# Performance work log

Measured on AMD Instinct MI355X. Metric: run time of the kernel, lower is better.

## Reference

```python
import jax, jax.numpy as jnp
import numpy as np

ROBOT_W = 1.0
PHASE_W = 1.0
COHER_W = 10.0
SPEED_W = 5.0
MAX_SPEED = 10.0
SMOOTH_VEL_W = 0.05
SMOOTH_ACC_W = 0.01

# illegal phase transitions {(0,2),(1,0),(2,0),(2,1)} as a 3x3 lookup table
_ILLEGAL = np.zeros((3, 3), dtype=bool)
for a, b in [(0, 2), (1, 0), (2, 0), (2, 1)]:
    _ILLEGAL[a, b] = True
ILLEGAL_TABLE = jnp.asarray(_ILLEGAL)


def setup_inputs() -> dict:
    key = jax.random.key(0)
    k1, k2, k3, k4 = jax.random.split(key, 4)
    B, T = 256, 8192
    # scale by 8 so per-frame speeds (norm of diffs of 3-vectors) exceed MAX_SPEED
    pred_robot = jax.random.normal(k1, (B, T, 12), dtype=jnp.float32) * 8.0
    gt_robot = jax.random.normal(k2, (B, T, 12), dtype=jnp.float32) * 8.0
    pred_phase = jax.random.normal(k3, (B, T, 3), dtype=jnp.float32)
    gt_phase = jax.random.randint(k4, (B, T), 0, 3, dtype=jnp.int32)
    return {"pred_robot": pred_robot, "pred_phase": pred_phase,
            "gt_robot": gt_robot, "gt_phase": gt_phase}


def _coherence_loss(phase_logits):
    # vectorized replacement for the O(B*T) Python double loop
    p = jnp.argmax(phase_logits, axis=-1)            # [B, T]
    pt, pt1 = p[:, :-1], p[:, 1:]                    # [B, T-1]
    illegal = ILLEGAL_TABLE[pt, pt1]                 # [B, T-1] bool
    # logit of the (illegal) predicted phase at t+1
    sel = jnp.take_along_axis(phase_logits[:, 1:], pt1[..., None], axis=-1)[..., 0]
    loss_sum = jnp.sum(jnp.where(illegal, sel * sel, 0.0))
    count = jnp.sum(illegal)
    return jnp.where(count > 0, loss_sum / jnp.maximum(count, 1).astype(sel.dtype), 0.0)


def _speed_loss(pred_robot):
    B, T, D = pred_robot.shape
    vel = pred_robot[:, 1:] - pred_robot[:, :-1]     # [B, T-1, 12]
    pts = vel.reshape(B, T - 1, 4, 3)
    speeds = jnp.linalg.norm(pts, axis=-1)           # [B, T-1, 4]
    pen = jax.nn.relu(speeds - MAX_SPEED)
    return SPEED_W * jnp.mean(pen * pen)


def reference(pred_robot, pred_phase, gt_robot, gt_phase):
    # MSE over robot trajectory
    robot_loss = jnp.mean((pred_robot - gt_robot) ** 2)
    # cross-entropy over 3 phase classes
    logp = jax.nn.log_softmax(pred_phase, axis=-1)   # [B, T, 3]
    nll = -jnp.take_along_axis(logp, gt_phase[..., None].astype(jnp.int32), axis=-1)[..., 0]
    phase_loss = jnp.mean(nll)
    coherence = _coherence_loss(pred_phase)
    speed_loss = _speed_loss(pred_robot)
    vel = pred_robot[:, 1:] - pred_robot[:, :-1]
    vel_loss = jnp.mean(vel * vel)
    acc = pred_robot[:, 2:] - 2.0 * pred_robot[:, 1:-1] + pred_robot[:, :-2]
    acc_loss = jnp.mean(acc * acc)
    total = (ROBOT_W * robot_loss + PHASE_W * phase_loss + COHER_W * coherence
             + speed_loss + SMOOTH_VEL_W * vel_loss + SMOOTH_ACC_W * acc_loss)
    return total
```

## Files before the change

### kernel.cpp

```cpp
#include <hip/hip_runtime.h>
#include <math.h>

#define B_DIM 256
#define T_DIM 8192
#define BLOCK 256
#define NSLOT 256
#define K_PRED 4
#define NPB (BLOCK * K_PRED)
#define NF4 (B_DIM * T_DIM * 3)
#define NPH4 (NF4 / 4)
#define GRID_BLOCKS (NF4 / NPB)


__device__ __forceinline__ unsigned div3u(unsigned x) {
    return __umulhi(x, 0xAAAAAAABu) >> 1;
}
__device__ __forceinline__ float pen_term(float s) {
    float d = fmaxf(sqrtf(s) - 10.0f, 0.0f);
    return d * d;
}
__device__ __forceinline__ void argmax3(float l0, float l1, float l2, int &p, float &m) {
    p = 0; m = l0;
    if (l1 > m) { m = l1; p = 1; }
    if (l2 > m) { m = l2; p = 2; }
}
__device__ __forceinline__ float nll3(float l0, float l1, float l2, int g) {
    float mx = fmaxf(l0, fmaxf(l1, l2));
    float lse = mx + logf(expf(l0 - mx) + expf(l1 - mx) + expf(l2 - mx));
    float sel = (g == 0) ? l0 : ((g == 1) ? l1 : l2);
    return lse - sel;
}

__global__ __launch_bounds__(BLOCK) void combined_loss_main(
    const float4* __restrict__ pred4,
    const float4* __restrict__ ph4,
    const float4* __restrict__ gt4,
    const int*    __restrict__ gt_phase,
    double* __restrict__ ws)
{
    __shared__ float  s_carry[NPB + 1];
    __shared__ float2 s_zw[BLOCK + 1];
    __shared__ float  s_pm_m[BLOCK + 1];
    __shared__ int    s_pm_p[BLOCK + 1];
    __shared__ float  s_red[4][6];

    const int tid = threadIdx.x;
    const int blk = blockIdx.x;
    const unsigned base = (unsigned)blk * NPB;

    float sse = 0.f, velsq = 0.f, accsq = 0.f;
    float loc[K_PRED], car[K_PRED];
    unsigned c0v = 0;

    #pragma unroll
    for (int k = 0; k < K_PRED; ++k) {
        const unsigned i = base + (unsigned)(k * BLOCK) + tid;
        const unsigned r = div3u(i);
        const unsigned c = i - 3u * r;
        if (k == 0) c0v = c;
        const unsigned t = r & (T_DIM - 1);
        const bool v1 = t < (T_DIM - 1);
        const bool v2 = t < (T_DIM - 2);
        const unsigned i3 = v1 ? i + 3u : i;
        const unsigned i6 = v2 ? i + 6u : i;

        const float4 A  = pred4[i];
        const float4 G  = gt4[i];
        const float4 A3 = pred4[i3];
        const float4 A6 = pred4[i6];

        float d;
        d = A.x - G.x; sse = fmaf(d, d, sse);
        d = A.y - G.y; sse = fmaf(d, d, sse);
        d = A.z - G.z; sse = fmaf(d, d, sse);
        d = A.w - G.w; sse = fmaf(d, d, sse);

        float sqx = 0.f, sqy = 0.f, sqz = 0.f, sqw = 0.f;
        if (v1) {
            const float vx = A3.x - A.x, vy = A3.y - A.y, vz = A3.z - A.z, vw = A3.w - A.w;
            sqx = vx * vx; sqy = vy * vy; sqz = vz * vz; sqw = vw * vw;
            velsq += sqx + sqy + sqz + sqw;
        }
        if (v2) {
            float a;
            a = A6.x - 2.0f * A3.x + A.x; accsq = fmaf(a, a, accsq);
            a = A6.y - 2.0f * A3.y + A.y; accsq = fmaf(a, a, accsq);
            a = A6.z - 2.0f * A3.z + A.z; accsq = fmaf(a, a, accsq);
            a = A6.w - 2.0f * A3.w + A.w; accsq = fmaf(a, a, accsq);
        }
        float l3v, crv;
        if (c == 0)      { l3v = sqx + sqy + sqz; crv = sqw; }
        else if (c == 1) { l3v = sqz + sqw;       crv = sqx + sqy; }
        else             { l3v = sqy + sqz + sqw; crv = sqx; }
        loc[k] = l3v; car[k] = crv;
        s_carry[k * BLOCK + tid] = crv;
    }

    const unsigned j = (unsigned)blk * BLOCK + tid;
    const float4 P = ph4[j];
    s_zw[tid + 1] = make_float2(P.z, P.w);

    if (tid == 0) {
        float2 zwp = make_float2(0.f, 0.f);
        if (j != 0) {
            const float2* ph2 = (const float2*)ph4;
            zwp = ph2[2u * j - 1u];
        }
        s_zw[0] = zwp;
        float crs = 0.f;
        const unsigned ib = base + NPB;
        if (ib < (unsigned)NF4) {
            const unsigned rb = div3u(ib);
            const unsigned cb = ib - 3u * rb;
            const unsigned tb = rb & (T_DIM - 1);
            if (tb < (T_DIM - 1)) {
                const float4 Ab  = pred4[ib];
                const float4 Ab3 = pred4[ib + 3u];
                const float bx = Ab3.x - Ab.x, by = Ab3.y - Ab.y;
                const float bz = Ab3.z - Ab.z, bw = Ab3.w - Ab.w;
                const float sx = bx * bx, sy = by * by, sx2 = bz * bz, sw = bw * bw;
                (void)sx2;
                crs = (cb == 0) ? sw : ((cb == 1) ? (sx + sy) : sx);
            }
        }
        s_carry[NPB] = crs;
    }
    __syncthreads();

    const unsigned g   = div3u(j);
    const unsigned dph = j - 3u * g;
    const float2 zwp = s_zw[tid];
    float l0, l1, l2;
    if (dph == 0)      { l0 = P.x;   l1 = P.y;   l2 = P.z; }
    else if (dph == 1) { l0 = zwp.y; l1 = P.x;   l2 = P.y; }
    else               { l0 = zwp.x; l1 = zwp.y; l2 = P.x; }
    const unsigned prow = 4u * g + dph;

    int gA, gB = 0;
    if (dph == 2) {
        const int2 gg = ((const int2*)gt_phase)[prow >> 1];
        gA = gg.x; gB = gg.y;
    } else {
        gA = gt_phase[prow];
    }
    float nll = nll3(l0, l1, l2, gA);
    int pP; float mP;
    argmax3(l0, l1, l2, pP, mP);
    s_pm_m[tid] = mP; s_pm_p[tid] = pP;

    int p3 = 0; float m3 = 0.f;
    if (dph == 2) {
        nll += nll3(P.y, P.z, P.w, gB);
        argmax3(P.y, P.z, P.w, p3, m3);
    }
    if (tid == BLOCK - 1) {
        float mS = 0.f; int pS = 0;
        const unsigned jn = j + 1u;
        if (jn < (unsigned)NPH4) {
            const float4 Pn = ph4[jn];
            const unsigned gn = div3u(jn);
            const unsigned dn = jn - 3u * gn;
            float a0, a1, a2;
            if (dn == 0)      { a0 = Pn.x; a1 = Pn.y; a2 = Pn.z; }
            else if (dn == 1) { a0 = P.w;  a1 = Pn.x; a2 = Pn.y; }
            else              { a0 = P.z;  a1 = P.w;  a2 = Pn.x; }
            argmax3(a0, a1, a2, pS, mS);
        }
        s_pm_m[BLOCK] = mS; s_pm_p[BLOCK] = pS;
    }
    __syncthreads();

    float csum = 0.f, ccnt = 0.f;
    {
        const float mN = s_pm_m[tid + 1];
        const int   pN = s_pm_p[tid + 1];
        const unsigned t1 = prow & (T_DIM - 1);
        if (t1 < (T_DIM - 1)) {
            const int   pB2 = (dph == 2) ? p3 : pN;
            const float mB2 = (dph == 2) ? m3 : mN;
            const int mask = (pP == 0) ? 4 : ((pP == 1) ? 1 : 3);
            if ((mask >> pB2) & 1) { csum += mB2 * mB2; ccnt += 1.f; }
        }
        if (dph == 2) {
            const unsigned t2 = (prow + 1u) & (T_DIM - 1);
            if (t2 < (T_DIM - 1)) {
                const int mask = (p3 == 0) ? 4 : ((p3 == 1) ? 1 : 3);
                if ((mask >> pN) & 1) { csum += mN * mN; ccnt += 1.f; }
            }
        }
    }

    float pen2 = 0.f;
    #pragma unroll
    for (int k = 0; k < K_PRED; ++k) {
        unsigned ck = c0v + (unsigned)k;
        if (ck >= 3u) ck -= 3u;
        const float up = s_carry[k * BLOCK + tid + 1];
        const float a = loc[k] + ((ck == 1u) ? up : 0.f);
        const float b = (ck == 0u) ? (car[k] + up) : 0.f;
        pen2 += pen_term(a) + pen_term(b);
    }

    float vals[6] = { fmaf(12.0f, nll, sse), csum, ccnt, pen2, velsq, accsq };
    #pragma unroll
    for (int off = 32; off > 0; off >>= 1) {
        #pragma unroll
        for (int q = 0; q < 6; ++q)
            vals[q] += __shfl_down(vals[q], off, 64);
    }
    const int wave = tid >> 6, lane = tid & 63;
    if (lane == 0) {
        #pragma unroll
        for (int q = 0; q < 6; ++q) s_red[wave][q] = vals[q];
    }
    __syncthreads();
    if (tid < 6) {
        const double acc = (double)s_red[0][tid] + (double)s_red[1][tid]
                         + (double)s_red[2][tid] + (double)s_red[3][tid];
        atomicAdd(&ws[(size_t)(blk & (NSLOT - 1)) * 8 + tid], acc);
    }
}

__global__ __launch_bounds__(256) void combined_loss_final(
    const double* __restrict__ ws, float* __restrict__ out)
{
    __shared__ double sred[4][6];
    const int tid = threadIdx.x;
    double v[6];
    #pragma unroll
    for (int q = 0; q < 6; ++q) v[q] = ws[(size_t)tid * 8 + q];
    #pragma unroll
    for (int off = 32; off > 0; off >>= 1) {
        #pragma unroll
        for (int q = 0; q < 6; ++q)
            v[q] += __shfl_down(v[q], off, 64);
    }
    const int wave = tid >> 6, lane = tid & 63;
    if (lane == 0) {
        #pragma unroll
        for (int q = 0; q < 6; ++q) sred[wave][q] = v[q];
    }
    __syncthreads();
    if (tid == 0) {
        double s[6];
        #pragma unroll
        for (int q = 0; q < 6; ++q)
            s[q] = sred[0][q] + sred[1][q] + sred[2][q] + sred[3][q];
        const double robot_phase = s[0] / (double)((size_t)B_DIM * T_DIM * 12);
        const double coher = (s[2] > 0.0) ? (s[1] / fmax(s[2], 1.0)) : 0.0;
        const double speed = 5.0  * (s[3] / (double)((size_t)B_DIM * (T_DIM - 1) * 4));
        const double vel   = 0.05 * (s[4] / (double)((size_t)B_DIM * (T_DIM - 1) * 12));
        const double acc   = 0.01 * (s[5] / (double)((size_t)B_DIM * (T_DIM - 2) * 12));
        out[0] = (float)(robot_phase + 10.0 * coher + speed + vel + acc);
    }
}

extern "C" void kernel_launch(void* const* d_in, const int* in_sizes, int n_in,
                              void* d_out, int out_size, void* d_ws, size_t ws_size,
                              hipStream_t stream)
{
    const float4* pred4      = (const float4*)d_in[0];
    const float4* ph4        = (const float4*)d_in[1];
    const float4* gt4        = (const float4*)d_in[2];
    const int*    gt_phase   = (const int*)d_in[3];
    double* ws  = (double*)d_ws;
    float*  out = (float*)d_out;

    hipMemsetAsync(d_ws, 0, (size_t)NSLOT * 8 * sizeof(double), stream);

    combined_loss_main<<<dim3(GRID_BLOCKS), BLOCK, 0, stream>>>(pred4, ph4, gt4, gt_phase, ws);
    combined_loss_final<<<1, 256, 0, stream>>>(ws, out);
}
```

Measured before the change: 241.9 us.

## Hoist all global loads ahead of compute and use fast exp/log intrinsics

Restructures the main kernel so every global load (prediction, ground truth, shifted neighbours, phase logits, boundary carry and next-phase values) is issued up front into register arrays before any arithmetic. This aims to increase memory-level parallelism and hide load latency. It also swaps expf/logf for __expf/__logf in the cross-entropy and adds a min-blocks-per-SM hint of 3 to launch_bounds. The cost is higher register pressure from holding 16 float4 values live, plus slightly lower precision in the log-sum-exp.

```diff
diff --git a/kernel.cpp b/kernel.cpp
--- a/kernel.cpp
+++ b/kernel.cpp
@@ -26,12 +26,12 @@
 }
 __device__ __forceinline__ float nll3(float l0, float l1, float l2, int g) {
     float mx = fmaxf(l0, fmaxf(l1, l2));
-    float lse = mx + logf(expf(l0 - mx) + expf(l1 - mx) + expf(l2 - mx));
+    float s = __expf(l0 - mx) + __expf(l1 - mx) + __expf(l2 - mx);
     float sel = (g == 0) ? l0 : ((g == 1) ? l1 : l2);
-    return lse - sel;
-}
-
-__global__ __launch_bounds__(BLOCK) void combined_loss_main(
+    return mx + __logf(s) - sel;
+}
+
+__global__ __launch_bounds__(BLOCK, 3) void combined_loss_main(
     const float4* __restrict__ pred4,
     const float4* __restrict__ ph4,
     const float4* __restrict__ gt4,
@@ -47,95 +47,54 @@
     const int tid = threadIdx.x;
     const int blk = blockIdx.x;
     const unsigned base = (unsigned)blk * NPB;
-
-    float sse = 0.f, velsq = 0.f, accsq = 0.f;
-    float loc[K_PRED], car[K_PRED];
-    unsigned c0v = 0;
-
+    const unsigned j = (unsigned)blk * BLOCK + tid;
+
+
+    float2 zwp_s = make_float2(0.f, 0.f);
+    float4 Ab = make_float4(0.f,0.f,0.f,0.f), Ab3 = Ab;
+    unsigned cb = 0; bool carry_sent = false;
+    if (tid == 0) {
+        if (j != 0) zwp_s = ((const float2*)ph4)[2u * j - 1u];
+        const unsigned ib = base + NPB;
+        if (ib < (unsigned)NF4) {
+            const unsigned rb = div3u(ib);
+            cb = ib - 3u * rb;
+            if ((rb & (T_DIM - 1)) < (T_DIM - 1)) {
+                carry_sent = true;
+                Ab  = pred4[ib];
+                Ab3 = pred4[ib + 3u];
+            }
+        }
+    }
+    float4 Pn = make_float4(0.f,0.f,0.f,0.f);
+    bool pn_valid = false;
+    if (tid == BLOCK - 1) {
+        if (j + 1u < (unsigned)NPH4) { pn_valid = true; Pn = ph4[j + 1u]; }
+    }
+
+    float4 A[K_PRED], G[K_PRED], A3[K_PRED], A6[K_PRED];
+    unsigned cc[K_PRED];
+    bool vv1[K_PRED], vv2[K_PRED];
     #pragma unroll
     for (int k = 0; k < K_PRED; ++k) {
         const unsigned i = base + (unsigned)(k * BLOCK) + tid;
         const unsigned r = div3u(i);
-        const unsigned c = i - 3u * r;
-        if (k == 0) c0v = c;
+        cc[k] = i - 3u * r;
         const unsigned t = r & (T_DIM - 1);
-        const bool v1 = t < (T_DIM - 1);
-        const bool v2 = t < (T_DIM - 2);
-        const unsigned i3 = v1 ? i + 3u : i;
-        const unsigned i6 = v2 ? i + 6u : i;
-
-        const float4 A  = pred4[i];
-        const float4 G  = gt4[i];
-        const float4 A3 = pred4[i3];
-        const float4 A6 = pred4[i6];
-
-        float d;
-        d = A.x - G.x; sse = fmaf(d, d, sse);
-        d = A.y - G.y; sse = fmaf(d, d, sse);
-        d = A.z - G.z; sse = fmaf(d, d, sse);
-        d = A.w - G.w; sse = fmaf(d, d, sse);
-
-        float sqx = 0.f, sqy = 0.f, sqz = 0.f, sqw = 0.f;
-        if (v1) {
-            const float vx = A3.x - A.x, vy = A3.y - A.y, vz = A3.z - A.z, vw = A3.w - A.w;
-            sqx = vx * vx; sqy = vy * vy; sqz = vz * vz; sqw = vw * vw;
-            velsq += sqx + sqy + sqz + sqw;
-        }
-        if (v2) {
-            float a;
-            a = A6.x - 2.0f * A3.x + A.x; accsq = fmaf(a, a, accsq);
-            a = A6.y - 2.0f * A3.y + A.y; accsq = fmaf(a, a, accsq);
-            a = A6.z - 2.0f * A3.z + A.z; accsq = fmaf(a, a, accsq);
-            a = A6.w - 2.0f * A3.w + A.w; accsq = fmaf(a, a, accsq);
-        }
-        float l3v, crv;
-        if (c == 0)      { l3v = sqx + sqy + sqz; crv = sqw; }
-        else if (c == 1) { l3v = sqz + sqw;       crv = sqx + sqy; }
-        else             { l3v = sqy + sqz + sqw; crv = sqx; }
-        loc[k] = l3v; car[k] = crv;
-        s_carry[k * BLOCK + tid] = crv;
-    }
-
-    const unsigned j = (unsigned)blk * BLOCK + tid;
+        vv1[k] = t < (T_DIM - 1);
+        vv2[k] = t < (T_DIM - 2);
+        const unsigned ia = vv1[k] ? i + 3u : i;
+        const unsigned ic = vv2[k] ? i + 6u : i;
+        A[k]  = pred4[i];
+        G[k]  = gt4[i];
+        A3[k] = pred4[ia];
+        A6[k] = pred4[ic];
+    }
+
     const float4 P = ph4[j];
-    s_zw[tid + 1] = make_float2(P.z, P.w);
-
-    if (tid == 0) {
-        float2 zwp = make_float2(0.f, 0.f);
-        if (j != 0) {
-            const float2* ph2 = (const float2*)ph4;
-            zwp = ph2[2u * j - 1u];
-        }
-        s_zw[0] = zwp;
-        float crs = 0.f;
-        const unsigned ib = base + NPB;
-        if (ib < (unsigned)NF4) {
-            const unsigned rb = div3u(ib);
-            const unsigned cb = ib - 3u * rb;
-            const unsigned tb = rb & (T_DIM - 1);
-            if (tb < (T_DIM - 1)) {
-                const float4 Ab  = pred4[ib];
-                const float4 Ab3 = pred4[ib + 3u];
-                const float bx = Ab3.x - Ab.x, by = Ab3.y - Ab.y;
-                const float bz = Ab3.z - Ab.z, bw = Ab3.w - Ab.w;
-                const float sx = bx * bx, sy = by * by, sx2 = bz * bz, sw = bw * bw;
-                (void)sx2;
-                crs = (cb == 0) ? sw : ((cb == 1) ? (sx + sy) : sx);
-            }
-        }
-        s_carry[NPB] = crs;
-    }
-    __syncthreads();
-
     const unsigned g   = div3u(j);
     const unsigned dph = j - 3u * g;
-    const float2 zwp = s_zw[tid];
-    float l0, l1, l2;
-    if (dph == 0)      { l0 = P.x;   l1 = P.y;   l2 = P.z; }
-    else if (dph == 1) { l0 = zwp.y; l1 = P.x;   l2 = P.y; }
-    else               { l0 = zwp.x; l1 = zwp.y; l2 = P.x; }
     const unsigned prow = 4u * g + dph;
-
     int gA, gB = 0;
     if (dph == 2) {
         const int2 gg = ((const int2*)gt_phase)[prow >> 1];
@@ -143,6 +102,62 @@
     } else {
         gA = gt_phase[prow];
     }
+
+
+    float sse = 0.f, velsq = 0.f, accsq = 0.f;
+    float loc[K_PRED], car[K_PRED];
+    #pragma unroll
+    for (int k = 0; k < K_PRED; ++k) {
+        float d;
+        d = A[k].x - G[k].x; sse = fmaf(d, d, sse);
+        d = A[k].y - G[k].y; sse = fmaf(d, d, sse);
+        d = A[k].z - G[k].z; sse = fmaf(d, d, sse);
+        d = A[k].w - G[k].w; sse = fmaf(d, d, sse);
+
+        float sqx = 0.f, sqy = 0.f, sqz = 0.f, sqw = 0.f;
+        if (vv1[k]) {
+            const float vx = A3[k].x - A[k].x, vy = A3[k].y - A[k].y;
+            const float vz = A3[k].z - A[k].z, vw = A3[k].w - A[k].w;
+            sqx = vx * vx; sqy = vy * vy; sqz = vz * vz; sqw = vw * vw;
+            velsq += sqx + sqy + sqz + sqw;
+        }
+        if (vv2[k]) {
+            float a;
+            a = A6[k].x - 2.0f * A3[k].x + A[k].x; accsq = fmaf(a, a, accsq);
+            a = A6[k].y - 2.0f * A3[k].y + A[k].y; accsq = fmaf(a, a, accsq);
+            a = A6[k].z - 2.0f * A3[k].z + A[k].z; accsq = fmaf(a, a, accsq);
+            a = A6[k].w - 2.0f * A3[k].w + A[k].w; accsq = fmaf(a, a, accsq);
+        }
+        float l3v, crv;
+        const unsigned c = cc[k];
+        if (c == 0)      { l3v = sqx + sqy + sqz; crv = sqw; }
+        else if (c == 1) { l3v = sqz + sqw;       crv = sqx + sqy; }
+        else             { l3v = sqy + sqz + sqw; crv = sqx; }
+        loc[k] = l3v; car[k] = crv;
+        s_carry[k * BLOCK + tid] = crv;
+    }
+
+    s_zw[tid + 1] = make_float2(P.z, P.w);
+    if (tid == 0) {
+        s_zw[0] = zwp_s;
+        float crs = 0.f;
+        if (carry_sent) {
+            const float bx = Ab3.x - Ab.x, by = Ab3.y - Ab.y;
+            const float bz = Ab3.z - Ab.z, bw = Ab3.w - Ab.w;
+            const float sx = bx * bx, sy = by * by, sw = bw * bw;
+            (void)bz;
+            crs = (cb == 0) ? sw : ((cb == 1) ? (sx + sy) : sx);
+        }
+        s_carry[NPB] = crs;
+    }
+    __syncthreads();
+
+    const float2 zwp = s_zw[tid];
+    float l0, l1, l2;
+    if (dph == 0)      { l0 = P.x;   l1 = P.y;   l2 = P.z; }
+    else if (dph == 1) { l0 = zwp.y; l1 = P.x;   l2 = P.y; }
+    else               { l0 = zwp.x; l1 = zwp.y; l2 = P.x; }
+
     float nll = nll3(l0, l1, l2, gA);
     int pP; float mP;
     argmax3(l0, l1, l2, pP, mP);
@@ -155,9 +170,8 @@
     }
     if (tid == BLOCK - 1) {
         float mS = 0.f; int pS = 0;
-        const unsigned jn = j + 1u;
-        if (jn < (unsigned)NPH4) {
-            const float4 Pn = ph4[jn];
+        if (pn_valid) {
+            const unsigned jn = j + 1u;
             const unsigned gn = div3u(jn);
             const unsigned dn = jn - 3u * gn;
             float a0, a1, a2;
@@ -193,8 +207,7 @@
     float pen2 = 0.f;
     #pragma unroll
     for (int k = 0; k < K_PRED; ++k) {
-        unsigned ck = c0v + (unsigned)k;
-        if (ck >= 3u) ck -= 3u;
+        unsigned ck = cc[k];
         const float up = s_carry[k * BLOCK + tid + 1];
         const float a = loc[k] + ((ck == 1u) ? up : 0.f);
         const float b = (ck == 0u) ? (car[k] + up) : 0.f;
```

Measured after the change: 239.4 us. About the same (-1.0%).
